# Optimization experiments

Measured on AMD Instinct MI355X. Metric: run time of the kernel, lower is better.

## Reference

```python
import jax, jax.numpy as jnp
import numpy as np

B, S, D = 2, 4096, 1024
H, W = 16, 128
HD = D // H  # 64


def setup_inputs() -> dict:
    key = jax.random.key(0)
    ks = jax.random.split(key, 6)
    x = jax.random.normal(ks[0], (B, S, D), dtype=jnp.float32)
    # standard RoPE angle table: theta[pos, i] = pos / 10000^(2i/hd)
    inv_freq = 1.0 / (10000.0 ** (jnp.arange(0, HD, 2, dtype=jnp.float32) / HD))  # (hd/2,)
    rope_freqs = jnp.arange(S, dtype=jnp.float32)[:, None] * inv_freq[None, :]     # (S, hd/2)
    scale = 0.02
    wq = jax.random.normal(ks[1], (D, D), dtype=jnp.float32) * scale
    wk = jax.random.normal(ks[2], (D, D), dtype=jnp.float32) * scale
    wv = jax.random.normal(ks[3], (D, D), dtype=jnp.float32) * scale
    wo = jax.random.normal(ks[4], (D, D), dtype=jnp.float32) * scale
    return {"x": x, "rope_freqs": rope_freqs, "wq": wq, "wk": wk, "wv": wv, "wo": wo}


def reference(x, rope_freqs, wq, wk, wv, wo):
    Bsz, Sl, Dm = x.shape
    hd = Dm // H
    q = (x @ wq.T).reshape(Bsz, Sl, H, hd)
    k = (x @ wk.T).reshape(Bsz, Sl, H, hd)
    v = (x @ wv.T).reshape(Bsz, Sl, H, hd)

    # rotate-half RoPE, angles broadcast over batch and heads
    f = rope_freqs[:Sl]                               # (S, hd/2)
    cos = jnp.cos(f)[None, :, None, :]
    sin = jnp.sin(f)[None, :, None, :]

    def rope(t):
        t1, t2 = jnp.split(t, 2, axis=-1)
        return jnp.concatenate([t1 * cos - t2 * sin, t2 * cos + t1 * sin], axis=-1)

    q = rope(q)
    k = rope(k)

    # block-local sliding-window attention: window [q-left, q+right]
    Bk = W                       # block size == window size
    nb = Sl // Bk                # S assumed divisible by W
    left = W // 2
    right = W - left - 1

    pad = [(0, 0), (Bk, Bk), (0, 0), (0, 0)]
    kb = jnp.pad(k, pad).reshape(Bsz, nb + 2, Bk, H, hd)
    vb = jnp.pad(v, pad).reshape(Bsz, nb + 2, Bk, H, hd)
    # each query block attends to 3 consecutive key blocks (prev, self, next)
    k3 = jnp.concatenate([kb[:, :-2], kb[:, 1:-1], kb[:, 2:]], axis=2)  # (B,nb,3Bk,H,hd)
    v3 = jnp.concatenate([vb[:, :-2], vb[:, 1:-1], vb[:, 2:]], axis=2)
    qb = q.reshape(Bsz, nb, Bk, H, hd)

    scale = 1.0 / jnp.sqrt(jnp.asarray(hd, dtype=x.dtype))
    scores = jnp.einsum('bnqhd,bnkhd->bnhqk', qb, k3) * scale  # (B,nb,H,Bk,3Bk)

    r = jnp.arange(Bk)
    c = jnp.arange(3 * Bk)
    rel = c[None, :] - Bk - r[:, None]                  # key_pos - query_pos, (Bk,3Bk)
    win = (rel >= -left) & (rel <= right)
    blk = jnp.arange(nb)
    key_pos = blk[:, None] * Bk + c[None, :] - Bk       # (nb,3Bk) absolute key positions
    valid = (key_pos >= 0) & (key_pos < Sl)
    mask = win[None, :, :] & valid[:, None, :]          # (nb,Bk,3Bk)

    scores = jnp.where(mask[None, :, None, :, :], scores, jnp.asarray(-1e30, scores.dtype))
    probs = jax.nn.softmax(scores, axis=-1)
    out = jnp.einsum('bnhqk,bnkhd->bnqhd', probs, v3).reshape(Bsz, Sl, H * hd)
    return out @ wo.T
```

## Files before the change

### kernel.cpp

```cpp
#include <hip/hip_runtime.h>

typedef unsigned short u16;
typedef unsigned int   u32;
typedef unsigned long long u64;
typedef __attribute__((ext_vector_type(4))) unsigned int u32x4;
typedef __attribute__((ext_vector_type(2))) unsigned int u32x2;
typedef __attribute__((ext_vector_type(8))) short        s16x8;
typedef __attribute__((ext_vector_type(4))) float        f32x4;
typedef __attribute__((ext_vector_type(2))) float        f32x2;

#define S_LEN 4096

typedef const __attribute__((address_space(1))) void gas_void;
typedef __attribute__((address_space(3))) void las_void;

__device__ __forceinline__ u16 f2bf(float f) {
    u32 u = __builtin_bit_cast(u32, f);
    u32 r = (u + 0x7fffu + ((u >> 16) & 1u)) >> 16;
    return (u16)r;
}

__device__ __forceinline__ float rmax16(float v) {
    v = fmaxf(v, __shfl_xor(v, 1));
    v = fmaxf(v, __shfl_xor(v, 2));
    v = fmaxf(v, __shfl_xor(v, 4));
    v = fmaxf(v, __shfl_xor(v, 8));
    return v;
}
__device__ __forceinline__ float rsum16(float v) {
    v += __shfl_xor(v, 1);
    v += __shfl_xor(v, 2);
    v += __shfl_xor(v, 4);
    v += __shfl_xor(v, 8);
    return v;
}

#define VMW0() asm volatile("s_waitcnt vmcnt(0)" ::: "memory")
#define VMWS(n) do { asm volatile("s_waitcnt vmcnt(" #n ")" ::: "memory"); \
                     __builtin_amdgcn_sched_barrier(0); } while (0)
#define SB0() __builtin_amdgcn_sched_barrier(0)
#define MFMA16(a, b, c) __builtin_amdgcn_mfma_f32_16x16x32_bf16(a, b, c, 0, 0, 0)
#define GL(p, d) __builtin_amdgcn_global_load_lds((gas_void*)(p), (las_void*)(d), 16, 0, 0)
#define GLB(d, a, o) asm volatile("global_load_dwordx4 %0, %1, off offset:" #o : "=v"(d) : "v"(a))

__global__ __launch_bounds__(256)
void prep_kernel(const float* __restrict__ x,
                 const float* __restrict__ wq, const float* __restrict__ wk,
                 const float* __restrict__ wv, const float* __restrict__ wo,
                 const float* __restrict__ freqs,
                 u16* __restrict__ apk, u16* __restrict__ bpk, u16* __restrict__ wopk,
                 float* __restrict__ tab) {
    const int bid = blockIdx.x;
    const int t   = threadIdx.x;
    if (bid >= 768) {
        const int i = (bid - 768) * 256 + t;
        const float f = freqs[i];
        float sn, cs;
        sincosf(f, &sn, &cs);
        tab[i * 2]     = cs;
        tab[i * 2 + 1] = sn;
        return;
    }
    __shared__ u16 L[16][1032];
    const float* src;
    u16* dst;
    int nft, frag0, rowblk;
    if (bid < 512) { src = x; dst = apk; nft = 512; rowblk = bid; frag0 = bid; }
    else {
        const int wsel = (bid - 512) >> 6;
        rowblk = (bid - 512) & 63;
        src = (wsel == 0) ? wq : (wsel == 1) ? wk : (wsel == 2) ? wv : wo;
        if (wsel < 3) { dst = bpk;  nft = 192; frag0 = wsel * 64 + rowblk; }
        else          { dst = wopk; nft = 64;  frag0 = rowblk; }
    }
#pragma unroll
    for (int r = 0; r < 16; ++r) {
        const f32x4 v = *(const f32x4*)(src + ((size_t)(rowblk * 16 + r)) * 1024 + t * 4);
        u16* Lp = &L[r][t * 4];
        Lp[0] = f2bf(v.x); Lp[1] = f2bf(v.y); Lp[2] = f2bf(v.z); Lp[3] = f2bf(v.w);
    }
    __syncthreads();
#pragma unroll
    for (int i = 0; i < 8; ++i) {
        const int idx = (i << 8) + t;
        const int c32 = idx >> 6;
        const int l   = idx & 63;
        const u32x4 d = *(const u32x4*)(&L[l & 15][(c32 << 5) + ((l >> 4) << 3)]);
        *(u32x4*)(dst + (((size_t)c32 * nft + frag0) * 64 + l) * 8) = d;
    }
}

#define FRAGS(P) s16x8 P##a0,P##a1,P##a2,P##a3, \
                       P##b0,P##b1,P##b2,P##b3,P##b4,P##b5,P##b6,P##b7

#define LD_TILE(P) do { \
    GLB(P##a0, aA, 0); GLB(P##a1, aA, 1024); GLB(P##a2, aA, 2048); GLB(P##a3, aA, 3072); \
    GLB(P##b0, aB0, 0); GLB(P##b1, aB0, 1024); GLB(P##b2, aB0, 2048); GLB(P##b3, aB0, 3072); \
    GLB(P##b4, aB1, 0); GLB(P##b5, aB1, 1024); GLB(P##b6, aB1, 2048); GLB(P##b7, aB1, 3072); \
    aA += 524288u; aB0 += (u64)SBK; aB1 += (u64)SBK; \
} while (0)

#define MFMA32P(P) do { \
    acc[0][0]=MFMA16(P##a0,P##b0,acc[0][0]); acc[1][0]=MFMA16(P##a1,P##b0,acc[1][0]); \
    acc[2][0]=MFMA16(P##a2,P##b0,acc[2][0]); acc[3][0]=MFMA16(P##a3,P##b0,acc[3][0]); \
    acc[0][1]=MFMA16(P##a0,P##b1,acc[0][1]); acc[1][1]=MFMA16(P##a1,P##b1,acc[1][1]); \
    acc[2][1]=MFMA16(P##a2,P##b1,acc[2][1]); acc[3][1]=MFMA16(P##a3,P##b1,acc[3][1]); \
    acc[0][2]=MFMA16(P##a0,P##b2,acc[0][2]); acc[1][2]=MFMA16(P##a1,P##b2,acc[1][2]); \
    acc[2][2]=MFMA16(P##a2,P##b2,acc[2][2]); acc[3][2]=MFMA16(P##a3,P##b2,acc[3][2]); \
    acc[0][3]=MFMA16(P##a0,P##b3,acc[0][3]); acc[1][3]=MFMA16(P##a1,P##b3,acc[1][3]); \
    acc[2][3]=MFMA16(P##a2,P##b3,acc[2][3]); acc[3][3]=MFMA16(P##a3,P##b3,acc[3][3]); \
    acc[0][4]=MFMA16(P##a0,P##b4,acc[0][4]); acc[1][4]=MFMA16(P##a1,P##b4,acc[1][4]); \
    acc[2][4]=MFMA16(P##a2,P##b4,acc[2][4]); acc[3][4]=MFMA16(P##a3,P##b4,acc[3][4]); \
    acc[0][5]=MFMA16(P##a0,P##b5,acc[0][5]); acc[1][5]=MFMA16(P##a1,P##b5,acc[1][5]); \
    acc[2][5]=MFMA16(P##a2,P##b5,acc[2][5]); acc[3][5]=MFMA16(P##a3,P##b5,acc[3][5]); \
    acc[0][6]=MFMA16(P##a0,P##b6,acc[0][6]); acc[1][6]=MFMA16(P##a1,P##b6,acc[1][6]); \
    acc[2][6]=MFMA16(P##a2,P##b6,acc[2][6]); acc[3][6]=MFMA16(P##a3,P##b6,acc[3][6]); \
    acc[0][7]=MFMA16(P##a0,P##b7,acc[0][7]); acc[1][7]=MFMA16(P##a1,P##b7,acc[1][7]); \
    acc[2][7]=MFMA16(P##a2,P##b7,acc[2][7]); acc[3][7]=MFMA16(P##a3,P##b7,acc[3][7]); \
} while (0)

template<int SBK, int MODE>
__global__ __launch_bounds__(256, 2)
void gemm_pk(const u16* __restrict__ Apk, const u16* __restrict__ Bpk,
             void* __restrict__ Cv, const float* __restrict__ cstab) {
    const int t    = threadIdx.x;
    const int bm   = blockIdx.x << 7;
    const int bn   = blockIdx.y << 8;
    const int wave = t >> 6;
    const int wr   = (wave >> 1) & 1;
    const int wc   = wave & 1;
    const int lane = t & 63;
    const int fr   = lane & 15;
    const int kg   = lane >> 4;

    u64 aA  = (u64)(uintptr_t)Apk + (u64)(((bm >> 4) + (wr << 2)) * 1024 + lane * 16);
    u64 aB0 = (u64)(uintptr_t)Bpk + (u64)(((bn >> 4) + (wc << 3)) * 1024 + lane * 16);
    u64 aB1 = aB0 + 4096u;

    f32x4 acc[4][8];
#pragma unroll
    for (int m = 0; m < 4; ++m)
#pragma unroll
        for (int n = 0; n < 8; ++n) acc[m][n] = f32x4{0.f, 0.f, 0.f, 0.f};

    FRAGS(X);
    FRAGS(Y);

    LD_TILE(X);
    LD_TILE(Y);

#pragma unroll 1
    for (int i = 0; i < 15; ++i) {
        VMWS(12);
        MFMA32P(X);
        SB0();
        LD_TILE(X);
        VMWS(12);
        MFMA32P(Y);
        SB0();
        LD_TILE(Y);
    }
    VMWS(12);
    MFMA32P(X);
    VMW0();
    SB0();
    MFMA32P(Y);

    if constexpr (MODE == 1) {
        const int sel   = bn >> 10;
        const int bcol  = (bn & 1023) + (wc << 7);
        const int crow0 = bm + (wr << 6) + (kg << 2);
        if (sel == 2) {
            u16* vt = (u16*)Cv + (size_t)16777216;
#pragma unroll
            for (int m = 0; m < 4; ++m) {
                const int row0 = crow0 + (m << 4);
                const int bb   = row0 >> 12;
                const int s0   = row0 & 4095;
#pragma unroll
                for (int nf = 0; nf < 8; ++nf) {
                    const int col = bcol + (nf << 4) + fr;
                    const int hh  = col >> 6;
                    const int d   = col & 63;
                    u32x2 pk;
                    pk.x = (u32)f2bf(acc[m][nf][0]) | ((u32)f2bf(acc[m][nf][1]) << 16);
                    pk.y = (u32)f2bf(acc[m][nf][2]) | ((u32)f2bf(acc[m][nf][3]) << 16);
                    *(u32x2*)(vt + ((size_t)((bb << 4) + hh) * 64 + d) * 4096 + s0) = pk;
                }
            }
        } else {
            u16* outb = (u16*)Cv + (size_t)sel * 8388608;
            const int hb = bcol >> 6;
#pragma unroll
            for (int m = 0; m < 4; ++m)
#pragma unroll
                for (int r = 0; r < 4; ++r) {
                    const int row = crow0 + (m << 4) + r;
                    const int s   = row & 4095;
                    const int bb  = row >> 12;
                    const f32x2 c0 = *(const f32x2*)(cstab + (((s << 5) + fr) << 1));
                    const f32x2 c1 = *(const f32x2*)(cstab + (((s << 5) + 16 + fr) << 1));
#pragma unroll
                    for (int g = 0; g < 2; ++g) {
                        u16* qp = outb + ((size_t)((bb << 4) + hb + g) * 4096 + s) * 64;
                        {
                            const float lo = acc[m][(g << 2) + 0][r];
                            const float hi = acc[m][(g << 2) + 2][r];
                            qp[fr]      = f2bf(lo * c0.x - hi * c0.y);
                            qp[32 + fr] = f2bf(hi * c0.x + lo * c0.y);
                        }
                        {
                            const float lo = acc[m][(g << 2) + 1][r];
                            const float hi = acc[m][(g << 2) + 3][r];
                            qp[16 + fr] = f2bf(lo * c1.x - hi * c1.y);
                            qp[48 + fr] = f2bf(hi * c1.x + lo * c1.y);
                        }
                    }
                }
        }
    } else {
        float* outf     = (float*)Cv;
        const int bcol  = bn + (wc << 7) + fr;
        const int crow0 = bm + (wr << 6) + (kg << 2);
#pragma unroll
        for (int m = 0; m < 4; ++m)
#pragma unroll
            for (int r = 0; r < 4; ++r) {
                const int row = crow0 + (m << 4) + r;
                float* op = outf + (size_t)row * 1024 + bcol;
#pragma unroll
                for (int nf = 0; nf < 8; ++nf)
                    op[nf << 4] = acc[m][nf][r];
            }
    }
}

__global__ __launch_bounds__(256)
void attn_kernel(const u16* __restrict__ Q, const u16* __restrict__ K,
                 const u16* __restrict__ Vt, u16* __restrict__ O) {
    __shared__ __align__(16) u16 Ks[192 * 64];
    __shared__ __align__(16) u16 Vs[64 * 192];
    const int bid0 = blockIdx.x;
    const int bid  = ((bid0 & 7) << 8) | (bid0 >> 3);
    const int ch  = bid & 63;
    const int h   = (bid >> 6) & 15;
    const int b   = bid >> 10;
    const int qs  = ch << 6;
    const int t   = threadIdx.x;
    const int ub  = t & 192;

    const u16* kwin = K + ((size_t)((b << 4) + h) << 18);

#pragma unroll
    for (int i = 0; i < 6; ++i) {
        const int cid = (i << 8) + t;
        const int row = cid >> 3;
        const int g   = (cid & 7) ^ (row & 7);
        const int kp  = qs - 64 + row;
        const u16* src = kwin + (long)kp * 64 + (g << 3);
        GL(src, &Ks[((i << 8) + ub) << 3]);
    }
#pragma unroll
    for (int i = 0; i < 6; ++i) {
        const int cid = (i << 8) + t;
        const int d   = cid / 24;
        const int c   = cid - d * 24;
        int g = c - (d & 7) * 3;
        if (g < 0) g += 24;
        const int key = qs - 64 + (g << 3);
        const u16* src = Vt + ((size_t)((b << 10) + (h << 6) + d)) * 4096 + key;
        GL(src, &Vs[((i << 8) + ub) << 3]);
    }

    const int w    = t >> 6;
    const int lane = t & 63;
    const int fr   = lane & 15;
    const int kg   = lane >> 4;
    const int f7   = fr & 7;

    const size_t qgoff = (((size_t)((b << 4) + h)) * 4096 + qs + (w << 4) + fr) * 64 + (kg << 3);
    const s16x8 qa0 = *(const s16x8*)(Q + qgoff);
    const s16x8 qa1 = *(const s16x8*)(Q + qgoff + 32);

    VMW0();
    __syncthreads();

    f32x4 sfr[9];
#pragma unroll
    for (int n = 0; n < 9; ++n) {
        const int row = (w << 4) + (n << 4) + fr;
        f32x4 a = f32x4{0.f, 0.f, 0.f, 0.f};
        const s16x8 kb0 = *(const s16x8*)(&Ks[(row << 6) + ((kg ^ f7) << 3)]);
        const s16x8 kb1 = *(const s16x8*)(&Ks[(row << 6) + (((4 + kg) ^ f7) << 3)]);
        a = MFMA16(qa0, kb0, a);
        a = MFMA16(qa1, kb1, a);
        sfr[n] = a;
    }

    const float NEG = -__builtin_inff();
    float mx[4] = {NEG, NEG, NEG, NEG};
#pragma unroll
    for (int n = 0; n < 9; ++n) {
        const int j = (n << 4) + fr;
#pragma unroll
        for (int r = 0; r < 4; ++r) {
            const int q  = (kg << 2) + r;
            const int kp = qs - 64 + (w << 4) + j;
            const bool valid = (j >= q) && (j - q < 128) && (kp >= 0) && (kp < S_LEN);
            const float s = valid ? sfr[n][r] * 0.125f : NEG;
            sfr[n][r] = s;
            mx[r] = fmaxf(mx[r], s);
        }
    }
#pragma unroll
    for (int r = 0; r < 4; ++r) mx[r] = rmax16(mx[r]);
    float ls[4] = {0.f, 0.f, 0.f, 0.f};
#pragma unroll
    for (int n = 0; n < 9; ++n)
#pragma unroll
        for (int r = 0; r < 4; ++r) {
            const float p = __expf(sfr[n][r] - mx[r]);
            sfr[n][r] = p;
            ls[r] += p;
        }
#pragma unroll
    for (int r = 0; r < 4; ++r) ls[r] = rsum16(ls[r]);

    __syncthreads();
    u16* Pw = Ks + w * 3072;
#pragma unroll
    for (int n = 0; n < 9; ++n) {
        const int j = (n << 4) + fr;
#pragma unroll
        for (int r = 0; r < 4; ++r) {
            const int q = (kg << 2) + r;
            Pw[q * 192 + (((j >> 3) ^ (q & 7)) << 3) + (j & 7)] = f2bf(sfr[n][r]);
        }
    }
    {
        const int j = 144 + fr;
#pragma unroll
        for (int r = 0; r < 4; ++r) {
            const int q = (kg << 2) + r;
            Pw[q * 192 + (((j >> 3) ^ (q & 7)) << 3) + (j & 7)] = 0;
        }
    }
    __syncthreads();

    f32x4 o[4];
#pragma unroll
    for (int nf = 0; nf < 4; ++nf) o[nf] = f32x4{0.f, 0.f, 0.f, 0.f};
    const int cs0 = f7 * 3;
#pragma unroll
    for (int ks = 0; ks < 5; ++ks) {
        const s16x8 pa = *(const s16x8*)(&Pw[fr * 192 + ((((ks << 2) + kg) ^ f7) << 3)]);
        int c = (w << 1) + (ks << 2) + kg;
        if (c > 23) c = 23;
        int cs = c + cs0;
        if (cs >= 24) cs -= 24;
#pragma unroll
        for (int nf = 0; nf < 4; ++nf) {
            const int d = (nf << 4) + fr;
            const s16x8 vbf = *(const s16x8*)(&Vs[d * 192 + (cs << 3)]);
            o[nf] = MFMA16(pa, vbf, o[nf]);
        }
    }

    const int mfrag = (b << 8) + (ch << 2) + w;
#pragma unroll
    for (int r = 0; r < 4; ++r) {
        const float inv = 1.f / ls[r];
#pragma unroll
        for (int nf = 0; nf < 4; ++nf) {
            const int kt  = (h << 1) + (nf >> 1);
            const int kgp = ((nf & 1) << 1) + (fr >> 3);
            const int lp  = (kgp << 4) + (kg << 2) + r;
            O[((((size_t)kt << 9) + mfrag) * 64 + lp) * 8 + (fr & 7)] = f2bf(o[nf][r] * inv);
        }
    }
}

extern "C" void kernel_launch(void* const* d_in, const int* in_sizes, int n_in,
                              void* d_out, int out_size, void* d_ws, size_t ws_size,
                              hipStream_t stream) {
    const float* x  = (const float*)d_in[0];
    const float* fr = (const float*)d_in[1];
    const float* wq = (const float*)d_in[2];
    const float* wk = (const float*)d_in[3];
    const float* wv = (const float*)d_in[4];
    const float* wo = (const float*)d_in[5];

    u16* ws    = (u16*)d_ws;
    u16* apk   = ws;
    u16* bpk   = apk + 8388608;
    u16* wopk  = bpk + 3145728;
    u16* qb    = wopk + 1048576;
    u16* kb    = qb + 8388608;
    u16* vtb   = kb + 8388608;
    float* cstab = (float*)(vtb + 8388608);
    u16* opk   = apk;

    prep_kernel<<<1280, 256, 0, stream>>>(x, wq, wk, wv, wo, fr, apk, bpk, wopk, cstab);

    dim3 gqkv(64, 12);
    gemm_pk<196608, 1><<<gqkv, 256, 0, stream>>>(apk, bpk, qb, cstab);

    attn_kernel<<<2048, 256, 0, stream>>>(qb, kb, vtb, opk);

    dim3 gout(64, 4);
    gemm_pk<65536, 2><<<gout, 256, 0, stream>>>(opk, wopk, (float*)d_out, nullptr);
}
```

Before: 109.1 us.

## Stage shared B tiles through LDS double buffer instead of per-wave global loads

The GEMM kernel now loads the B operand once per workgroup into a double-buffered LDS tile via global_load_lds, and each wave reads its B fragments from LDS with ds_read_b128. Before, the two waves sharing a column half each fetched the same B fragments from global memory. A operands still stream directly into registers. MFMA blocks are wrapped in s_setprio raises. This cuts redundant global/L2 traffic for B, at the cost of workgroup barriers each k-step and 32KB of LDS per block, which may affect occupancy and add sync stalls.

Measured after the change: 106.6 us. 2.3% less time.

```diff
diff --git a/kernel.cpp b/kernel.cpp
--- a/kernel.cpp
+++ b/kernel.cpp
@@ -38,7 +38,11 @@
 #define VMW0() asm volatile("s_waitcnt vmcnt(0)" ::: "memory")
 #define VMWS(n) do { asm volatile("s_waitcnt vmcnt(" #n ")" ::: "memory"); \
                      __builtin_amdgcn_sched_barrier(0); } while (0)
+#define LGKM0() do { asm volatile("s_waitcnt lgkmcnt(0)" ::: "memory"); \
+                     __builtin_amdgcn_sched_barrier(0); } while (0)
 #define SB0() __builtin_amdgcn_sched_barrier(0)
+#define DSR0(d, a)   asm volatile("ds_read_b128 %0, %1"              : "=v"(d) : "v"(a))
+#define DSR(d, a, o) asm volatile("ds_read_b128 %0, %1 offset:" #o   : "=v"(d) : "v"(a))
 #define MFMA16(a, b, c) __builtin_amdgcn_mfma_f32_16x16x32_bf16(a, b, c, 0, 0, 0)
 #define GL(p, d) __builtin_amdgcn_global_load_lds((gas_void*)(p), (las_void*)(d), 16, 0, 0)
 #define GLB(d, a, o) asm volatile("global_load_dwordx4 %0, %1, off offset:" #o : "=v"(d) : "v"(a))
@@ -93,14 +97,27 @@
 #define FRAGS(P) s16x8 P##a0,P##a1,P##a2,P##a3, \
                        P##b0,P##b1,P##b2,P##b3,P##b4,P##b5,P##b6,P##b7
 
-#define LD_TILE(P) do { \
+#define LDA(P) do { \
     GLB(P##a0, aA, 0); GLB(P##a1, aA, 1024); GLB(P##a2, aA, 2048); GLB(P##a3, aA, 3072); \
-    GLB(P##b0, aB0, 0); GLB(P##b1, aB0, 1024); GLB(P##b2, aB0, 2048); GLB(P##b3, aB0, 3072); \
-    GLB(P##b4, aB1, 0); GLB(P##b5, aB1, 1024); GLB(P##b6, aB1, 2048); GLB(P##b7, aB1, 3072); \
-    aA += 524288u; aB0 += (u64)SBK; aB1 += (u64)SBK; \
+    aA += 524288u; \
 } while (0)
 
+#define SGB(BUF) do { \
+    GL((const u16*)gBs,          &Bs[BUF][(((wave << 2) + 0) << 9)]); \
+    GL((const u16*)(gBs + 1024), &Bs[BUF][(((wave << 2) + 1) << 9)]); \
+    GL((const u16*)(gBs + 2048), &Bs[BUF][(((wave << 2) + 2) << 9)]); \
+    GL((const u16*)(gBs + 3072), &Bs[BUF][(((wave << 2) + 3) << 9)]); \
+    gBs += (u64)SBK; \
+} while (0)
+
+#define LDB(P, BUF) do { \
+    const u32 rb_ = ldsB + ((BUF) ? 16384u : 0u) + (wc << 13) + (lane << 4); \
+    DSR0(P##b0, rb_); DSR(P##b1, rb_, 1024); DSR(P##b2, rb_, 2048); DSR(P##b3, rb_, 3072); \
+    DSR(P##b4, rb_, 4096); DSR(P##b5, rb_, 5120); DSR(P##b6, rb_, 6144); DSR(P##b7, rb_, 7168); \
+} while (0)
+
 #define MFMA32P(P) do { \
+    __builtin_amdgcn_s_setprio(1); \
     acc[0][0]=MFMA16(P##a0,P##b0,acc[0][0]); acc[1][0]=MFMA16(P##a1,P##b0,acc[1][0]); \
     acc[2][0]=MFMA16(P##a2,P##b0,acc[2][0]); acc[3][0]=MFMA16(P##a3,P##b0,acc[3][0]); \
     acc[0][1]=MFMA16(P##a0,P##b1,acc[0][1]); acc[1][1]=MFMA16(P##a1,P##b1,acc[1][1]); \
@@ -117,12 +134,14 @@
     acc[2][6]=MFMA16(P##a2,P##b6,acc[2][6]); acc[3][6]=MFMA16(P##a3,P##b6,acc[3][6]); \
     acc[0][7]=MFMA16(P##a0,P##b7,acc[0][7]); acc[1][7]=MFMA16(P##a1,P##b7,acc[1][7]); \
     acc[2][7]=MFMA16(P##a2,P##b7,acc[2][7]); acc[3][7]=MFMA16(P##a3,P##b7,acc[3][7]); \
+    __builtin_amdgcn_s_setprio(0); \
 } while (0)
 
 template<int SBK, int MODE>
 __global__ __launch_bounds__(256, 2)
-void gemm_pk(const u16* __restrict__ Apk, const u16* __restrict__ Bpk,
+void gemm_hy(const u16* __restrict__ Apk, const u16* __restrict__ Bpk,
              void* __restrict__ Cv, const float* __restrict__ cstab) {
+    __shared__ __align__(1024) u16 Bs[2][8192];
     const int t    = threadIdx.x;
     const int bm   = blockIdx.x << 7;
     const int bn   = blockIdx.y << 8;
@@ -133,9 +152,9 @@
     const int fr   = lane & 15;
     const int kg   = lane >> 4;
 
-    u64 aA  = (u64)(uintptr_t)Apk + (u64)(((bm >> 4) + (wr << 2)) * 1024 + lane * 16);
-    u64 aB0 = (u64)(uintptr_t)Bpk + (u64)(((bn >> 4) + (wc << 3)) * 1024 + lane * 16);
-    u64 aB1 = aB0 + 4096u;
+    u64 aA  = (u64)(uintptr_t)Apk + (u64)((((bm >> 4) + (wr << 2)) << 10) + (lane << 4));
+    u64 gBs = (u64)(uintptr_t)Bpk + (u64)((((bn >> 4) + (wave << 2)) << 10) + (lane << 4));
+    const u32 ldsB = (u32)(size_t)(las_void*)&Bs[0][0];
 
     f32x4 acc[4][8];
 #pragma unroll
@@ -146,22 +165,37 @@
     FRAGS(X);
     FRAGS(Y);
 
-    LD_TILE(X);
-    LD_TILE(Y);
+    SGB(0);
+    LDA(X);
+    SGB(1);
+    LDA(Y);
+    VMWS(12);
+    __builtin_amdgcn_s_barrier();
+    LDB(X, 0);
 
 #pragma unroll 1
-    for (int i = 0; i < 15; ++i) {
-        VMWS(12);
+    for (int jj = 0; jj < 15; ++jj) {
+        LGKM0();
+        VMWS(4);
+        __builtin_amdgcn_s_barrier();
+        SGB(0);
+        LDB(Y, 1);
         MFMA32P(X);
-        SB0();
-        LD_TILE(X);
-        VMWS(12);
+        LDA(X);
+        LGKM0();
+        VMWS(4);
+        __builtin_amdgcn_s_barrier();
+        SGB(1);
+        LDB(X, 0);
         MFMA32P(Y);
-        SB0();
-        LD_TILE(Y);
-    }
-    VMWS(12);
+        LDA(Y);
+    }
+    LGKM0();
+    VMWS(4);
+    __builtin_amdgcn_s_barrier();
+    LDB(Y, 1);
     MFMA32P(X);
+    LGKM0();
     VMW0();
     SB0();
     MFMA32P(Y);
@@ -403,10 +437,10 @@
     prep_kernel<<<1280, 256, 0, stream>>>(x, wq, wk, wv, wo, fr, apk, bpk, wopk, cstab);
 
     dim3 gqkv(64, 12);
-    gemm_pk<196608, 1><<<gqkv, 256, 0, stream>>>(apk, bpk, qb, cstab);
+    gemm_hy<196608, 1><<<gqkv, 256, 0, stream>>>(apk, bpk, qb, cstab);
 
     attn_kernel<<<2048, 256, 0, stream>>>(qb, kb, vtb, opk);
 
     dim3 gout(64, 4);
-    gemm_pk<65536, 2><<<gout, 256, 0, stream>>>(opk, wopk, (float*)d_out, nullptr);
-}
+    gemm_hy<65536, 2><<<gout, 256, 0, stream>>>(opk, wopk, (float*)d_out, nullptr);
+}
```
